# Kernel tuning notes

Measured on AMD Instinct MI355X. Metric: run time of the kernel, lower is better.

The kernel has to match this reference:

```python
import jax, jax.numpy as jnp
import numpy as np

RETRIEVAL_TEMP = 0.5
TOP_K = 50


def setup_inputs() -> dict:
    key = jax.random.key(0)
    ks = jax.random.split(key, 8)
    B, N, D = 64, 50000, 2048
    return {
        "query_vec": jax.random.normal(ks[0], (B, D), dtype=jnp.float32),
        "vritti_types": jax.random.randint(ks[1], (N,), 0, 5, dtype=jnp.int64),
        "seed_memory": jax.random.normal(ks[2], (N, D), dtype=jnp.float32) * 0.02,
        "karma_scores": jax.random.normal(ks[3], (N,), dtype=jnp.float32) * 0.1,
        "vritti_bias": jnp.array([0.15, 0.1, -0.05, 0.0, -1.0], dtype=jnp.float32),
        "W1": jax.random.normal(ks[4], (D, 2 * D), dtype=jnp.float32) * (1.0 / np.sqrt(D)),
        "b1": jnp.zeros((2 * D,), dtype=jnp.float32),
        "W2": jax.random.normal(ks[5], (2 * D, D), dtype=jnp.float32) * (1.0 / np.sqrt(2 * D)),
        "b2": jnp.zeros((D,), dtype=jnp.float32),
    }


def reference(query_vec, vritti_types, seed_memory, karma_scores, vritti_bias, W1, b1, W2, b2):
    # Query MLP: Linear -> GELU (exact, erf-based, torch default) -> Linear
    h = jax.nn.gelu(query_vec @ W1 + b1, approximate=False)      # [B, 2D]
    q = h @ W2 + b2                                              # [B, D]
    # Similarity against the full seed bank
    sims = jnp.einsum("bd,nd->bn", q, seed_memory)               # [B, N]
    # Karma gating (elementwise, broadcast over batch)
    karma_gate = jax.nn.sigmoid((karma_scores + 0.3) * 10.0)     # [N]
    sims = sims * karma_gate[None, :]
    # Per-seed vritti bias (gather from 5-entry table)
    sims = sims + vritti_bias[vritti_types][None, :]
    # Temperature softmax over all seeds
    attention_weights = jax.nn.softmax(sims / RETRIEVAL_TEMP, axis=-1)  # [B, N]
    # Top-k retrieval (sorted descending, matches torch.topk)
    topk_values, topk_indices = jax.lax.top_k(attention_weights, TOP_K)  # [B, K]
    # Vectorized per-batch gather of retrieved seed embeddings
    chitta_field = seed_memory[topk_indices]                     # [B, K, D]
    return (chitta_field, attention_weights, topk_indices)
```

## Files before the change

### kernel.cpp

```cpp
#include <hip/hip_runtime.h>
#include <math.h>

#define B 64
#define D 2048
#define H 4096
#define NSEED 50000
#define KTOP 50
#define NCAND 64
#define CEMIT 20
#define NCHUNKS 64
#define CHUNK_SZ 782

#define WS_LOGITS   0
#define WS_H        3200000
#define WS_Q2       (WS_H + B*H)
#define WS_PART     (WS_Q2 + B*D)
#define WS_CVAL     (WS_PART + 1048576)
#define WS_CIDX     (WS_CVAL + 262144)
#define WS_CM       (WS_CIDX + 262144)
#define WS_CS       (WS_CM + 4096)
#define WS_RM       (WS_CS + 4096)
#define WS_RS       (WS_RM + 64)
#define WS_Q2HL     (WS_RS + 64)
#define WSP_CAND    200000
#define WSP_RVAL    220000
#define WSP_TIDX    240000

typedef short s16x8 __attribute__((ext_vector_type(8)));
typedef float f32x4 __attribute__((ext_vector_type(4)));

__device__ __forceinline__ unsigned short bf16_rne(float x)
{
    unsigned int b = __float_as_uint(x);
    b += 0x7FFFu + ((b >> 16) & 1u);
    return (unsigned short)(b >> 16);
}
__device__ __forceinline__ float bf16_tof(unsigned short h)
{
    return __uint_as_float(((unsigned int)h) << 16);
}

__global__ __launch_bounds__(256) void gemm64p_kernel(
    const float* __restrict__ A, const float* __restrict__ W,
    float* __restrict__ part, int K, int N, int kcK, int nBlocks)
{
    __shared__ float As[2][32][68];
    __shared__ float Bs[2][32][68];

    const int tid = threadIdx.x;
    const int nb = blockIdx.x % nBlocks;
    const int kc = blockIdx.x / nBlocks;
    const int kbeg = kc * kcK;

    const int tidm = tid >> 4;
    const int tidn = tid & 15;
    const int m0 = tidm * 4;
    const int n0 = tidn * 4;

    const int ar0 = tid >> 3, ac0 = tid & 7;
    const int wr0 = tid >> 4, wc0 = tid & 15;

    const float* Aptr0 = A + (size_t)ar0 * K + kbeg + ac0 * 4;
    const float* Aptr1 = A + (size_t)(ar0 + 32) * K + kbeg + ac0 * 4;
    const float* Wptr0 = W + (size_t)(kbeg + wr0) * N + nb * 64 + wc0 * 4;
    const float* Wptr1 = W + (size_t)(kbeg + wr0 + 16) * N + nb * 64 + wc0 * 4;

    float acc[4][4];
#pragma unroll
    for (int i = 0; i < 4; ++i)
#pragma unroll
        for (int j = 0; j < 4; ++j) acc[i][j] = 0.f;

    float4 pa0 = *(const float4*)(Aptr0);
    float4 pa1 = *(const float4*)(Aptr1);
    float4 pb0 = *(const float4*)(Wptr0);
    float4 pb1 = *(const float4*)(Wptr1);

    const int nsteps = kcK / 32;
    for (int s = 0; s < nsteps; ++s) {
        const int buf = s & 1;
        As[buf][ac0 * 4 + 0][ar0] = pa0.x;
        As[buf][ac0 * 4 + 1][ar0] = pa0.y;
        As[buf][ac0 * 4 + 2][ar0] = pa0.z;
        As[buf][ac0 * 4 + 3][ar0] = pa0.w;
        As[buf][ac0 * 4 + 0][ar0 + 32] = pa1.x;
        As[buf][ac0 * 4 + 1][ar0 + 32] = pa1.y;
        As[buf][ac0 * 4 + 2][ar0 + 32] = pa1.z;
        As[buf][ac0 * 4 + 3][ar0 + 32] = pa1.w;
        *(float4*)&Bs[buf][wr0][wc0 * 4] = pb0;
        *(float4*)&Bs[buf][wr0 + 16][wc0 * 4] = pb1;
        if (s + 1 < nsteps) {
            const int ko = 32 * (s + 1);
            pa0 = *(const float4*)(Aptr0 + ko);
            pa1 = *(const float4*)(Aptr1 + ko);
            pb0 = *(const float4*)(Wptr0 + (size_t)ko * N);
            pb1 = *(const float4*)(Wptr1 + (size_t)ko * N);
        }
        __syncthreads();
#pragma unroll
        for (int kk = 0; kk < 32; ++kk) {
            float4 a = *(const float4*)&As[buf][kk][m0];
            float4 b = *(const float4*)&Bs[buf][kk][n0];
            float av[4] = {a.x, a.y, a.z, a.w};
            float bv[4] = {b.x, b.y, b.z, b.w};
#pragma unroll
            for (int i = 0; i < 4; ++i)
#pragma unroll
                for (int j = 0; j < 4; ++j)
                    acc[i][j] += av[i] * bv[j];
        }
    }

#pragma unroll
    for (int i = 0; i < 4; ++i) {
        float4 v;
        v.x = acc[i][0]; v.y = acc[i][1]; v.z = acc[i][2]; v.w = acc[i][3];
        *(float4*)(part + (size_t)(kc * B + m0 + i) * N + nb * 64 + n0) = v;
    }
}

__global__ void mlp_reduce_kernel(const float* __restrict__ part,
                                  const float* __restrict__ bias,
                                  float* __restrict__ out, int N, int nchunks, int gelu,
                                  unsigned short* __restrict__ uh,
                                  unsigned short* __restrict__ ul)
{
    int e = blockIdx.x * 256 + threadIdx.x;
    int b = e / N, j = e - b * N;
    float s = bias[j];
    for (int c = 0; c < nchunks; ++c)
        s += part[(size_t)(c * B + b) * N + j];
    if (gelu)
        s = 0.5f * s * (1.0f + erff(s * 0.70710678118654752f));
    out[e] = s;
    if (uh) {
        unsigned short h = bf16_rne(s);
        uh[e] = h;
        ul[e] = bf16_rne(s - bf16_tof(h));
    }
}

__device__ __forceinline__ bool types_is_i64(const int* t)
{
    int acc = 0;
#pragma unroll
    for (int j = 0; j < 16; ++j) acc |= t[2 * j + 1];
    return acc == 0;
}

__global__ __launch_bounds__(256, 4) void sims_mfma_kernel(
    const unsigned short* __restrict__ q2h, const unsigned short* __restrict__ q2l,
    const float* __restrict__ seed,
    const float* __restrict__ karma, const int* __restrict__ types,
    const float* __restrict__ vbias, float* __restrict__ logits)
{
    __shared__ __align__(16) unsigned short Ash[2][64][72];
    __shared__ __align__(16) unsigned short Asl[2][64][72];

    const int tid = threadIdx.x;
    const int n0 = blockIdx.x * 64;
    const int lane = tid & 63;
    const int wv  = tid >> 6;
    const int l15 = lane & 15;
    const int lg  = lane >> 4;

    const int srow = tid >> 2;
    const int seg  = tid & 3;

    const int nrow = n0 + wv * 16 + l15;
    const bool nvalid = nrow < NSEED;
    const float* brow = seed + (size_t)nrow * D + 8 * lg;
    const size_t aoff = (size_t)srow * D + 16 * seg;

    f32x4 acc[4];
#pragma unroll
    for (int t = 0; t < 4; ++t) acc[t] = (f32x4){0.f, 0.f, 0.f, 0.f};

    s16x8 aha, ahb, ala, alb;
    float4 b00, b01, b02, b03;
    float4 b10, b11, b12, b13;

    aha = *(const s16x8*)(q2h + aoff);
    ahb = *(const s16x8*)(q2h + aoff + 8);
    ala = *(const s16x8*)(q2l + aoff);
    alb = *(const s16x8*)(q2l + aoff + 8);
    b00 = b01 = b02 = b03 = make_float4(0.f, 0.f, 0.f, 0.f);
    b10 = b11 = b12 = b13 = make_float4(0.f, 0.f, 0.f, 0.f);
    if (nvalid) {
        b00 = *(const float4*)(brow);      b01 = *(const float4*)(brow + 4);
        b02 = *(const float4*)(brow + 32); b03 = *(const float4*)(brow + 36);
        b10 = *(const float4*)(brow + 64); b11 = *(const float4*)(brow + 68);
        b12 = *(const float4*)(brow + 96); b13 = *(const float4*)(brow + 100);
    }

#define SIMS_BARRIER() asm volatile("s_waitcnt lgkmcnt(0)\n\ts_barrier" ::: "memory")

#define SIMS_CONV(F0, F1, BH, BL)                                          \
    {                                                                      \
        union { unsigned int w[4]; s16x8 v; } uh_, ul_;                    \
        float xs[8] = {F0.x, F0.y, F0.z, F0.w, F1.x, F1.y, F1.z, F1.w};    \
        _Pragma("unroll")                                                  \
        for (int j = 0; j < 4; ++j) {                                      \
            unsigned int u0 = __float_as_uint(xs[2 * j]);                  \
            unsigned int u1 = __float_as_uint(xs[2 * j + 1]);              \
            unsigned int h0 = u0 & 0xFFFF0000u;                            \
            unsigned int h1 = u1 & 0xFFFF0000u;                            \
            uh_.w[j] = (u0 >> 16) | h1;                                    \
            float r0 = xs[2 * j]     - __uint_as_float(h0);                \
            float r1 = xs[2 * j + 1] - __uint_as_float(h1);                \
            ul_.w[j] = (__float_as_uint(r0) >> 16)                         \
                     | (__float_as_uint(r1) & 0xFFFF0000u);                \
        }                                                                  \
        BH = uh_.v; BL = ul_.v;                                            \
    }

#define SIMS_MFMA(BUF, KS, BH, BL)                                         \
    _Pragma("unroll")                                                      \
    for (int t = 0; t < 4; ++t) {                                          \
        s16x8 ah = *(const s16x8*)&Ash[BUF][t * 16 + l15][KS * 32 + 8 * lg]; \
        s16x8 al = *(const s16x8*)&Asl[BUF][t * 16 + l15][KS * 32 + 8 * lg]; \
        acc[t] = __builtin_amdgcn_mfma_f32_16x16x32_bf16(ah, BH, acc[t], 0, 0, 0); \
        acc[t] = __builtin_amdgcn_mfma_f32_16x16x32_bf16(al, BH, acc[t], 0, 0, 0); \
        acc[t] = __builtin_amdgcn_mfma_f32_16x16x32_bf16(ah, BL, acc[t], 0, 0, 0); \
    }

    for (int u = 0; u < 16; ++u) {
        *(s16x8*)&Ash[0][srow][16 * seg]     = aha;
        *(s16x8*)&Ash[0][srow][16 * seg + 8] = ahb;
        *(s16x8*)&Asl[0][srow][16 * seg]     = ala;
        *(s16x8*)&Asl[0][srow][16 * seg + 8] = alb;
        {
            const int kb = 128 * u + 64;
            aha = *(const s16x8*)(q2h + aoff + kb);
            ahb = *(const s16x8*)(q2h + aoff + kb + 8);
            ala = *(const s16x8*)(q2l + aoff + kb);
            alb = *(const s16x8*)(q2l + aoff + kb + 8);
        }
        float4 n0a = make_float4(0.f, 0.f, 0.f, 0.f), n0b = n0a, n0c = n0a, n0d = n0a;
        if (u < 15 && nvalid) {
            const int kb = 128 * u + 128;
            n0a = *(const float4*)(brow + kb);      n0b = *(const float4*)(brow + kb + 4);
            n0c = *(const float4*)(brow + kb + 32); n0d = *(const float4*)(brow + kb + 36);
        }
        SIMS_BARRIER();
        {
            s16x8 bh, bl;
            SIMS_CONV(b00, b01, bh, bl);
            SIMS_MFMA(0, 0, bh, bl);
            SIMS_CONV(b02, b03, bh, bl);
            SIMS_MFMA(0, 1, bh, bl);
        }
        b00 = n0a; b01 = n0b; b02 = n0c; b03 = n0d;

        *(s16x8*)&Ash[1][srow][16 * seg]     = aha;
        *(s16x8*)&Ash[1][srow][16 * seg + 8] = ahb;
        *(s16x8*)&Asl[1][srow][16 * seg]     = ala;
        *(s16x8*)&Asl[1][srow][16 * seg + 8] = alb;
        if (u < 15) {
            const int kb = 128 * u + 128;
            aha = *(const s16x8*)(q2h + aoff + kb);
            ahb = *(const s16x8*)(q2h + aoff + kb + 8);
            ala = *(const s16x8*)(q2l + aoff + kb);
            alb = *(const s16x8*)(q2l + aoff + kb + 8);
        }
        float4 n1a = make_float4(0.f, 0.f, 0.f, 0.f), n1b = n1a, n1c = n1a, n1d = n1a;
        if (u < 15 && nvalid) {
            const int kb = 128 * u + 192;
            n1a = *(const float4*)(brow + kb);      n1b = *(const float4*)(brow + kb + 4);
            n1c = *(const float4*)(brow + kb + 32); n1d = *(const float4*)(brow + kb + 36);
        }
        SIMS_BARRIER();
        {
            s16x8 bh, bl;
            SIMS_CONV(b10, b11, bh, bl);
            SIMS_MFMA(1, 0, bh, bl);
            SIMS_CONV(b12, b13, bh, bl);
            SIMS_MFMA(1, 1, bh, bl);
        }
        b10 = n1a; b11 = n1b; b12 = n1c; b13 = n1d;
    }
#undef SIMS_CONV
#undef SIMS_MFMA
#undef SIMS_BARRIER

    if (nvalid) {
        const bool i64 = types_is_i64(types);
        float ka = karma[nrow];
        float gate = 1.0f / (1.0f + expf(-(ka + 0.3f) * 10.0f));
        int ty = i64 ? types[2 * nrow] : types[nrow];
        float bias = vbias[ty];
#pragma unroll
        for (int t = 0; t < 4; ++t) {
#pragma unroll
            for (int r = 0; r < 4; ++r) {
                int m = t * 16 + lg * 4 + r;
                logits[(size_t)m * NSEED + nrow] = acc[t][r] * gate + bias;
            }
        }
    }
}

__global__ __launch_bounds__(64) void chunk_topk_kernel(
    const float* __restrict__ logits,
    float* __restrict__ chunk_m, float* __restrict__ chunk_s,
    float* __restrict__ cand_val, int* __restrict__ cand_idx)
{
    const int bid = blockIdx.x;
    const int row = bid >> 6, chunk = bid & 63;
    const int start = chunk * CHUNK_SZ;
    const int end = min(start + CHUNK_SZ, NSEED);
    const int lane = threadIdx.x;
    const float* Lrow = logits + (size_t)row * NSEED;

    float v[13];
#pragma unroll
    for (int j = 0; j < 13; ++j) {
        int e = start + lane + j * 64;
        v[j] = (e < end) ? Lrow[e] : -INFINITY;
    }

    float m = v[0];
#pragma unroll
    for (int j = 1; j < 13; ++j) m = fmaxf(m, v[j]);
    float s = 0.f;
#pragma unroll
    for (int j = 0; j < 13; ++j) s += expf(2.f * (v[j] - m));
#pragma unroll
    for (int d = 1; d < 64; d <<= 1) {
        float mo = __shfl_xor(m, d);
        float so = __shfl_xor(s, d);
        float nm = fmaxf(m, mo);
        s = s * expf(2.f * (m - nm)) + so * expf(2.f * (mo - nm));
        m = nm;
    }
    if (lane == 0) { chunk_m[bid] = m; chunk_s[bid] = s; }

    for (int it = 0; it < CEMIT; ++it) {
        float bv = v[0]; int bj = 0;
#pragma unroll
        for (int j = 1; j < 13; ++j)
            if (v[j] > bv) { bv = v[j]; bj = j; }
        int bi = start + lane + bj * 64;
#pragma unroll
        for (int d = 1; d < 64; d <<= 1) {
            float ov = __shfl_xor(bv, d);
            int oi = __shfl_xor(bi, d);
            if (ov > bv || (ov == bv && oi < bi)) { bv = ov; bi = oi; }
        }
        if (lane == 0) {
            cand_val[bid * CEMIT + it] = bv;
            cand_idx[bid * CEMIT + it] = bi;
        }
#pragma unroll
        for (int j = 0; j < 13; ++j)
            if (start + lane + j * 64 == bi) v[j] = -INFINITY;
    }
}

__global__ __launch_bounds__(256) void merge_topk_kernel(
    const float* __restrict__ chunk_m, const float* __restrict__ chunk_s,
    const float* __restrict__ cand_val, const int* __restrict__ cand_idx,
    float* __restrict__ row_M, float* __restrict__ row_rS,
    int* __restrict__ cand2)
{
    const int row = blockIdx.x;
    const int tid = threadIdx.x;
    const int lane = tid & 63, wave = tid >> 6;
    __shared__ float rv[4];
    __shared__ int ri[4];

    if (wave == 0) {
        float m = chunk_m[row * 64 + lane];
        float s = chunk_s[row * 64 + lane];
#pragma unroll
        for (int d = 1; d < 64; d <<= 1) {
            float mo = __shfl_xor(m, d);
            float so = __shfl_xor(s, d);
            float nm = fmaxf(m, mo);
            s = s * expf(2.f * (m - nm)) + so * expf(2.f * (mo - nm));
            m = nm;
        }
        if (lane == 0) { row_M[row] = m; row_rS[row] = 1.0f / s; }
    }

    float v[5]; int ix[5];
#pragma unroll
    for (int j = 0; j < 5; ++j) {
        int e = tid + j * 256;
        v[j] = cand_val[row * (NCHUNKS * CEMIT) + e];
        ix[j] = cand_idx[row * (NCHUNKS * CEMIT) + e];
    }

    for (int it = 0; it < NCAND; ++it) {
        float bv = v[0]; int bi = ix[0];
#pragma unroll
        for (int j = 1; j < 5; ++j)
            if (v[j] > bv || (v[j] == bv && ix[j] < bi)) { bv = v[j]; bi = ix[j]; }
#pragma unroll
        for (int d = 1; d < 64; d <<= 1) {
            float ov = __shfl_xor(bv, d);
            int oi = __shfl_xor(bi, d);
            if (ov > bv || (ov == bv && oi < bi)) { bv = ov; bi = oi; }
        }
        if (lane == 0) { rv[wave] = bv; ri[wave] = bi; }
        __syncthreads();
        float wv = rv[0]; int wi = ri[0];
#pragma unroll
        for (int w = 1; w < 4; ++w)
            if (rv[w] > wv || (rv[w] == wv && ri[w] < wi)) { wv = rv[w]; wi = ri[w]; }
        __syncthreads();
        if (tid == 0) cand2[row * NCAND + it] = wi;
#pragma unroll
        for (int j = 0; j < 5; ++j)
            if (ix[j] == wi) v[j] = -INFINITY;
    }
}

__global__ __launch_bounds__(256) void rescore_kernel(
    const float* __restrict__ q2, const float* __restrict__ seed,
    const float* __restrict__ karma, const int* __restrict__ types,
    const float* __restrict__ vbias, const int* __restrict__ cand2,
    float* __restrict__ rvals)
{
    const int row = blockIdx.y;
    const int wv = threadIdx.x >> 6, lane = threadIdx.x & 63;
    const int ci = blockIdx.x * 4 + wv;
    const int idx = cand2[row * NCAND + ci];
    const float* qrow = q2 + (size_t)row * D;
    const float* srow = seed + (size_t)idx * D;

    double s = 0.0;
#pragma unroll
    for (int i = 0; i < 8; ++i) {
        float4 a = *(const float4*)(qrow + lane * 4 + i * 256);
        float4 b = *(const float4*)(srow + lane * 4 + i * 256);
        s += (double)a.x * (double)b.x + (double)a.y * (double)b.y
           + (double)a.z * (double)b.z + (double)a.w * (double)b.w;
    }
#pragma unroll
    for (int d = 1; d < 64; d <<= 1) s += __shfl_xor(s, d);

    if (lane == 0) {
        float ka = karma[idx];
        float gate = 1.0f / (1.0f + expf(-(ka + 0.3f) * 10.0f));
        bool i64 = types_is_i64(types);
        int ty = i64 ? types[2 * idx] : types[idx];
        rvals[row * NCAND + ci] = (float)s * gate + vbias[ty];
    }
}

__global__ __launch_bounds__(64) void final50_kernel(
    const float* __restrict__ rvals, const int* __restrict__ cand2,
    float* __restrict__ out_idx_f, int* __restrict__ topk_idx)
{
    const int row = blockIdx.x;
    const int lane = threadIdx.x;

    float v = rvals[row * NCAND + lane];
    int ix = cand2[row * NCAND + lane];

    for (int it = 0; it < KTOP; ++it) {
        float bv = v; int bi = ix;
#pragma unroll
        for (int d = 1; d < 64; d <<= 1) {
            float ov = __shfl_xor(bv, d);
            int oi = __shfl_xor(bi, d);
            if (ov > bv || (ov == bv && oi < bi)) { bv = ov; bi = oi; }
        }
        if (lane == 0) {
            out_idx_f[row * KTOP + it] = (float)bi;
            topk_idx[row * KTOP + it] = bi;
        }
        if (ix == bi) v = -INFINITY;
    }
}

__global__ void weights_kernel(const float* __restrict__ logits,
                               const float* __restrict__ row_M,
                               const float* __restrict__ row_rS,
                               float* __restrict__ attn)
{
    const int row = blockIdx.y;
    const int f = blockIdx.x * 256 + threadIdx.x;
    if (f >= NSEED / 4) return;
    const float M = row_M[row], rS = row_rS[row];
    float4 l = ((const float4*)(logits + (size_t)row * NSEED))[f];
    float4 w;
    w.x = expf(2.f * (l.x - M)) * rS;
    w.y = expf(2.f * (l.y - M)) * rS;
    w.z = expf(2.f * (l.z - M)) * rS;
    w.w = expf(2.f * (l.w - M)) * rS;
    ((float4*)(attn + (size_t)row * NSEED))[f] = w;
}

__global__ void gather_kernel(const float* __restrict__ seed,
                              const int* __restrict__ topk_idx,
                              float* __restrict__ chitta)
{
    const int k = blockIdx.x, row = blockIdx.y;
    const int idx = topk_idx[row * KTOP + k];
    const float4* src = (const float4*)(seed + (size_t)idx * D);
    float4* dst = (float4*)(chitta + (size_t)(row * KTOP + k) * D);
#pragma unroll
    for (int j = 0; j < 2; ++j)
        dst[threadIdx.x + j * 256] = src[threadIdx.x + j * 256];
}

extern "C" void kernel_launch(void* const* d_in, const int* in_sizes, int n_in,
                              void* d_out, int out_size, void* d_ws, size_t ws_size,
                              hipStream_t stream)
{
    const float* query = (const float*)d_in[0];
    const int*   types = (const int*)d_in[1];
    const float* seed  = (const float*)d_in[2];
    const float* karma = (const float*)d_in[3];
    const float* vbias = (const float*)d_in[4];
    const float* W1    = (const float*)d_in[5];
    const float* b1    = (const float*)d_in[6];
    const float* W2    = (const float*)d_in[7];
    const float* b2    = (const float*)d_in[8];

    float* ws = (float*)d_ws;
    float* logits = ws + WS_LOGITS;
    float* h      = ws + WS_H;
    float* q2     = ws + WS_Q2;
    float* part   = ws + WS_PART;
    float* cval   = ws + WS_CVAL;
    int*   cidx   = (int*)(ws + WS_CIDX);
    float* cm     = ws + WS_CM;
    float* cs     = ws + WS_CS;
    float* rM     = ws + WS_RM;
    float* rS     = ws + WS_RS;

    unsigned short* q2h = (unsigned short*)(ws + WS_Q2HL);
    unsigned short* q2l = q2h + (size_t)B * D;

    int*   cand2 = (int*)(part + WSP_CAND);
    float* rvals = part + WSP_RVAL;
    int*   tidx  = (int*)(part + WSP_TIDX);

    float* outv   = (float*)d_out;
    float* chitta = outv;
    float* attn   = outv + (size_t)B * KTOP * D;
    float* oidxf  = attn + (size_t)B * NSEED;

    gemm64p_kernel<<<64 * 8, 256, 0, stream>>>(query, W1, logits, D, H, 256, 64);
    mlp_reduce_kernel<<<(B * H) / 256, 256, 0, stream>>>(logits, b1, h, H, 8, 1, nullptr, nullptr);
    gemm64p_kernel<<<32 * 8, 256, 0, stream>>>(h, W2, logits, H, D, 512, 32);
    mlp_reduce_kernel<<<(B * D) / 256, 256, 0, stream>>>(logits, b2, q2, D, 8, 0, q2h, q2l);
    sims_mfma_kernel<<<(NSEED + 63) / 64, 256, 0, stream>>>(q2h, q2l, seed, karma, types, vbias, logits);
    chunk_topk_kernel<<<B * NCHUNKS, 64, 0, stream>>>(logits, cm, cs, cval, cidx);
    merge_topk_kernel<<<B, 256, 0, stream>>>(cm, cs, cval, cidx, rM, rS, cand2);
    rescore_kernel<<<dim3(NCAND / 4, B), 256, 0, stream>>>(q2, seed, karma, types, vbias, cand2, rvals);
    final50_kernel<<<B, 64, 0, stream>>>(rvals, cand2, oidxf, tidx);
    weights_kernel<<<dim3((NSEED / 4 + 255) / 256, B), 256, 0, stream>>>(logits, rM, rS, attn);
    gather_kernel<<<dim3(KTOP, B), 256, 0, stream>>>(seed, tidx, chitta);
}
```

Measured before the change: 318.1 us.

## Fuse merge/rescore/final top-k kernels and weights+gather; add MFMA priority hints

```diff
diff --git a/kernel.cpp b/kernel.cpp
--- a/kernel.cpp
+++ b/kernel.cpp
@@ -10,6 +10,7 @@
 #define CEMIT 20
 #define NCHUNKS 64
 #define CHUNK_SZ 782
+#define WBLK ((NSEED / 4 + 255) / 256)
 
 #define WS_LOGITS   0
 #define WS_H        3200000
@@ -22,8 +23,6 @@
 #define WS_RM       (WS_CS + 4096)
 #define WS_RS       (WS_RM + 64)
 #define WS_Q2HL     (WS_RS + 64)
-#define WSP_CAND    200000
-#define WSP_RVAL    220000
 #define WSP_TIDX    240000
 
 typedef short s16x8 __attribute__((ext_vector_type(8)));
@@ -215,6 +214,7 @@
     }
 
 #define SIMS_MFMA(BUF, KS, BH, BL)                                         \
+    __builtin_amdgcn_s_setprio(1);                                         \
     _Pragma("unroll")                                                      \
     for (int t = 0; t < 4; ++t) {                                          \
         s16x8 ah = *(const s16x8*)&Ash[BUF][t * 16 + l15][KS * 32 + 8 * lg]; \
@@ -222,7 +222,8 @@
         acc[t] = __builtin_amdgcn_mfma_f32_16x16x32_bf16(ah, BH, acc[t], 0, 0, 0); \
         acc[t] = __builtin_amdgcn_mfma_f32_16x16x32_bf16(al, BH, acc[t], 0, 0, 0); \
         acc[t] = __builtin_amdgcn_mfma_f32_16x16x32_bf16(ah, BL, acc[t], 0, 0, 0); \
-    }
+    }                                                                      \
+    __builtin_amdgcn_s_setprio(0);
 
     for (int u = 0; u < 16; ++u) {
         *(s16x8*)&Ash[0][srow][16 * seg]     = aha;
@@ -357,17 +358,22 @@
     }
 }
 
-__global__ __launch_bounds__(256) void merge_topk_kernel(
+__global__ __launch_bounds__(256) void fused_topk_kernel(
     const float* __restrict__ chunk_m, const float* __restrict__ chunk_s,
     const float* __restrict__ cand_val, const int* __restrict__ cand_idx,
+    const float* __restrict__ q2, const float* __restrict__ seed,
+    const float* __restrict__ karma, const int* __restrict__ types,
+    const float* __restrict__ vbias,
     float* __restrict__ row_M, float* __restrict__ row_rS,
-    int* __restrict__ cand2)
+    float* __restrict__ out_idx_f, int* __restrict__ topk_idx)
 {
     const int row = blockIdx.x;
     const int tid = threadIdx.x;
     const int lane = tid & 63, wave = tid >> 6;
     __shared__ float rv[4];
     __shared__ int ri[4];
+    __shared__ int   c2s[NCAND];
+    __shared__ float rvs[NCAND];
 
     if (wave == 0) {
         float m = chunk_m[row * 64 + lane];
@@ -390,7 +396,6 @@
         v[j] = cand_val[row * (NCHUNKS * CEMIT) + e];
         ix[j] = cand_idx[row * (NCHUNKS * CEMIT) + e];
     }
-
     for (int it = 0; it < NCAND; ++it) {
         float bv = v[0]; int bi = ix[0];
 #pragma unroll
@@ -409,101 +414,86 @@
         for (int w = 1; w < 4; ++w)
             if (rv[w] > wv || (rv[w] == wv && ri[w] < wi)) { wv = rv[w]; wi = ri[w]; }
         __syncthreads();
-        if (tid == 0) cand2[row * NCAND + it] = wi;
+        if (tid == 0) c2s[it] = wi;
 #pragma unroll
         for (int j = 0; j < 5; ++j)
             if (ix[j] == wi) v[j] = -INFINITY;
     }
-}
-
-__global__ __launch_bounds__(256) void rescore_kernel(
-    const float* __restrict__ q2, const float* __restrict__ seed,
-    const float* __restrict__ karma, const int* __restrict__ types,
-    const float* __restrict__ vbias, const int* __restrict__ cand2,
-    float* __restrict__ rvals)
-{
-    const int row = blockIdx.y;
-    const int wv = threadIdx.x >> 6, lane = threadIdx.x & 63;
-    const int ci = blockIdx.x * 4 + wv;
-    const int idx = cand2[row * NCAND + ci];
+    __syncthreads();
+
+    const bool i64 = types_is_i64(types);
     const float* qrow = q2 + (size_t)row * D;
-    const float* srow = seed + (size_t)idx * D;
-
-    double s = 0.0;
-#pragma unroll
-    for (int i = 0; i < 8; ++i) {
-        float4 a = *(const float4*)(qrow + lane * 4 + i * 256);
-        float4 b = *(const float4*)(srow + lane * 4 + i * 256);
-        s += (double)a.x * (double)b.x + (double)a.y * (double)b.y
-           + (double)a.z * (double)b.z + (double)a.w * (double)b.w;
-    }
-#pragma unroll
-    for (int d = 1; d < 64; d <<= 1) s += __shfl_xor(s, d);
-
-    if (lane == 0) {
-        float ka = karma[idx];
-        float gate = 1.0f / (1.0f + expf(-(ka + 0.3f) * 10.0f));
-        bool i64 = types_is_i64(types);
-        int ty = i64 ? types[2 * idx] : types[idx];
-        rvals[row * NCAND + ci] = (float)s * gate + vbias[ty];
-    }
-}
-
-__global__ __launch_bounds__(64) void final50_kernel(
-    const float* __restrict__ rvals, const int* __restrict__ cand2,
-    float* __restrict__ out_idx_f, int* __restrict__ topk_idx)
-{
-    const int row = blockIdx.x;
-    const int lane = threadIdx.x;
-
-    float v = rvals[row * NCAND + lane];
-    int ix = cand2[row * NCAND + lane];
-
-    for (int it = 0; it < KTOP; ++it) {
-        float bv = v; int bi = ix;
-#pragma unroll
-        for (int d = 1; d < 64; d <<= 1) {
-            float ov = __shfl_xor(bv, d);
-            int oi = __shfl_xor(bi, d);
-            if (ov > bv || (ov == bv && oi < bi)) { bv = ov; bi = oi; }
-        }
+    for (int ci = wave; ci < NCAND; ci += 4) {
+        const int idx = c2s[ci];
+        const float* srow = seed + (size_t)idx * D;
+        double s = 0.0;
+#pragma unroll
+        for (int i = 0; i < 8; ++i) {
+            float4 a = *(const float4*)(qrow + lane * 4 + i * 256);
+            float4 b = *(const float4*)(srow + lane * 4 + i * 256);
+            s += (double)a.x * (double)b.x + (double)a.y * (double)b.y
+               + (double)a.z * (double)b.z + (double)a.w * (double)b.w;
+        }
+#pragma unroll
+        for (int d = 1; d < 64; d <<= 1) s += __shfl_xor(s, d);
         if (lane == 0) {
-            out_idx_f[row * KTOP + it] = (float)bi;
-            topk_idx[row * KTOP + it] = bi;
-        }
-        if (ix == bi) v = -INFINITY;
-    }
-}
-
-__global__ void weights_kernel(const float* __restrict__ logits,
-                               const float* __restrict__ row_M,
-                               const float* __restrict__ row_rS,
-                               float* __restrict__ attn)
-{
-    const int row = blockIdx.y;
-    const int f = blockIdx.x * 256 + threadIdx.x;
-    if (f >= NSEED / 4) return;
-    const float M = row_M[row], rS = row_rS[row];
-    float4 l = ((const float4*)(logits + (size_t)row * NSEED))[f];
-    float4 w;
-    w.x = expf(2.f * (l.x - M)) * rS;
-    w.y = expf(2.f * (l.y - M)) * rS;
-    w.z = expf(2.f * (l.z - M)) * rS;
-    w.w = expf(2.f * (l.w - M)) * rS;
-    ((float4*)(attn + (size_t)row * NSEED))[f] = w;
-}
-
-__global__ void gather_kernel(const float* __restrict__ seed,
-                              const int* __restrict__ topk_idx,
-                              float* __restrict__ chitta)
-{
-    const int k = blockIdx.x, row = blockIdx.y;
-    const int idx = topk_idx[row * KTOP + k];
-    const float4* src = (const float4*)(seed + (size_t)idx * D);
-    float4* dst = (float4*)(chitta + (size_t)(row * KTOP + k) * D);
-#pragma unroll
-    for (int j = 0; j < 2; ++j)
-        dst[threadIdx.x + j * 256] = src[threadIdx.x + j * 256];
+            float ka = karma[idx];
+            float gate = 1.0f / (1.0f + expf(-(ka + 0.3f) * 10.0f));
+            int ty = i64 ? types[2 * idx] : types[idx];
+            rvs[ci] = (float)s * gate + vbias[ty];
+        }
+    }
+    __syncthreads();
+
+    if (wave == 0) {
+        float fv = rvs[lane];
+        int fx = c2s[lane];
+        for (int it = 0; it < KTOP; ++it) {
+            float bv = fv; int bi = fx;
+#pragma unroll
+            for (int d = 1; d < 64; d <<= 1) {
+                float ov = __shfl_xor(bv, d);
+                int oi = __shfl_xor(bi, d);
+                if (ov > bv || (ov == bv && oi < bi)) { bv = ov; bi = oi; }
+            }
+            if (lane == 0) {
+                out_idx_f[row * KTOP + it] = (float)bi;
+                topk_idx[row * KTOP + it] = bi;
+            }
+            if (fx == bi) fv = -INFINITY;
+        }
+    }
+}
+
+__global__ __launch_bounds__(256) void weights_gather_kernel(
+    const float* __restrict__ logits, const float* __restrict__ row_M,
+    const float* __restrict__ row_rS, const float* __restrict__ seed,
+    const int* __restrict__ topk_idx,
+    float* __restrict__ attn, float* __restrict__ chitta)
+{
+    const int bid = blockIdx.x;
+    if (bid < WBLK * B) {
+        const int row = bid / WBLK, fb = bid - row * WBLK;
+        const int f = fb * 256 + threadIdx.x;
+        if (f >= NSEED / 4) return;
+        const float M = row_M[row], rS = row_rS[row];
+        float4 l = ((const float4*)(logits + (size_t)row * NSEED))[f];
+        float4 w;
+        w.x = expf(2.f * (l.x - M)) * rS;
+        w.y = expf(2.f * (l.y - M)) * rS;
+        w.z = expf(2.f * (l.z - M)) * rS;
+        w.w = expf(2.f * (l.w - M)) * rS;
+        ((float4*)(attn + (size_t)row * NSEED))[f] = w;
+    } else {
+        const int b2 = bid - WBLK * B;
+        const int row = b2 / KTOP, k = b2 - row * KTOP;
+        const int idx = topk_idx[row * KTOP + k];
+        const float4* src = (const float4*)(seed + (size_t)idx * D);
+        float4* dst = (float4*)(chitta + (size_t)(row * KTOP + k) * D);
+#pragma unroll
+        for (int j = 0; j < 2; ++j)
+            dst[threadIdx.x + j * 256] = src[threadIdx.x + j * 256];
+    }
 }
 
 extern "C" void kernel_launch(void* const* d_in, const int* in_sizes, int n_in,
@@ -535,9 +525,7 @@
     unsigned short* q2h = (unsigned short*)(ws + WS_Q2HL);
     unsigned short* q2l = q2h + (size_t)B * D;
 
-    int*   cand2 = (int*)(part + WSP_CAND);
-    float* rvals = part + WSP_RVAL;
-    int*   tidx  = (int*)(part + WSP_TIDX);
+    int* tidx = (int*)(part + WSP_TIDX);
 
     float* outv   = (float*)d_out;
     float* chitta = outv;
@@ -550,9 +538,8 @@
     mlp_reduce_kernel<<<(B * D) / 256, 256, 0, stream>>>(logits, b2, q2, D, 8, 0, q2h, q2l);
     sims_mfma_kernel<<<(NSEED + 63) / 64, 256, 0, stream>>>(q2h, q2l, seed, karma, types, vbias, logits);
     chunk_topk_kernel<<<B * NCHUNKS, 64, 0, stream>>>(logits, cm, cs, cval, cidx);
-    merge_topk_kernel<<<B, 256, 0, stream>>>(cm, cs, cval, cidx, rM, rS, cand2);
-    rescore_kernel<<<dim3(NCAND / 4, B), 256, 0, stream>>>(q2, seed, karma, types, vbias, cand2, rvals);
-    final50_kernel<<<B, 64, 0, stream>>>(rvals, cand2, oidxf, tidx);
-    weights_kernel<<<dim3((NSEED / 4 + 255) / 256, B), 256, 0, stream>>>(logits, rM, rS, attn);
-    gather_kernel<<<dim3(KTOP, B), 256, 0, stream>>>(seed, tidx, chitta);
-}
+    fused_topk_kernel<<<B, 256, 0, stream>>>(cm, cs, cval, cidx, q2, seed, karma, types, vbias,
+                                             rM, rS, oidxf, tidx);
+    weights_gather_kernel<<<WBLK * B + B * KTOP, 256, 0, stream>>>(
+        logits, rM, rS, seed, tidx, attn, chitta);
+}
```

Result: slower. 361.7 us (+13.7%).
